# Kernel tuning notes

Hardware: AMD Instinct MI355X
Metric: run time of the kernel (lower is better)

Reference implementation:

```python
import jax, jax.numpy as jnp
import numpy as np

D_MODEL = 1024
NUM_HEADS = 16
NUM_KV_HEADS = 4
D_K = D_MODEL // NUM_HEADS  # 64
GROUP = NUM_HEADS // NUM_KV_HEADS  # 4
ROPE_BASE = 10000.0
NEG = -10000.0


def _rope_cos_sin(seq_len, d_k, dtype):
    # matches standard RotaryEmbedding: inv_freq over even dims, emb = cat(freqs, freqs)
    inv_freq = 1.0 / (ROPE_BASE ** (jnp.arange(0, d_k, 2, dtype=jnp.float32) / d_k))
    t = jnp.arange(seq_len, dtype=jnp.float32)
    freqs = jnp.einsum('s,f->sf', t, inv_freq)          # [S, d_k/2]
    emb = jnp.concatenate([freqs, freqs], axis=-1)       # [S, d_k]
    return jnp.cos(emb).astype(dtype), jnp.sin(emb).astype(dtype)


def _apply_rope(x, cos, sin):
    # x: [B, H, S, d_k]; cos/sin: [S, d_k] broadcast over B, H
    half = x.shape[-1] // 2
    x1, x2 = x[..., :half], x[..., half:]
    rotated = jnp.concatenate([-x2, x1], axis=-1)
    return x * cos + rotated * sin


def setup_inputs() -> dict:
    key = jax.random.key(0)
    ks = jax.random.split(key, 7)
    B, S = 2, 2048
    scale = 1.0 / np.sqrt(D_MODEL)
    return {
        'query': jax.random.normal(ks[0], (B, S, D_MODEL), dtype=jnp.float32),
        'key': jax.random.normal(ks[1], (B, S, D_MODEL), dtype=jnp.float32),
        'value': jax.random.normal(ks[2], (B, S, D_MODEL), dtype=jnp.float32),
        'Wq': jax.random.normal(ks[3], (D_MODEL, D_MODEL), dtype=jnp.float32) * scale,
        'Wk': jax.random.normal(ks[4], (NUM_KV_HEADS * D_K, D_MODEL), dtype=jnp.float32) * scale,
        'Wv': jax.random.normal(ks[5], (NUM_KV_HEADS * D_K, D_MODEL), dtype=jnp.float32) * scale,
        'Wo': jax.random.normal(ks[6], (D_MODEL, D_MODEL), dtype=jnp.float32) * scale,
    }


def reference(query, key, value, Wq, Wk, Wv, Wo):
    B, Sq, _ = query.shape
    Sk = key.shape[1]
    # projections (nn.Linear: x @ W.T)
    Q = (query @ Wq.T).reshape(B, Sq, NUM_HEADS, D_K).transpose(0, 2, 1, 3)      # [B,H,Sq,dk]
    K = (key @ Wk.T).reshape(B, Sk, NUM_KV_HEADS, D_K).transpose(0, 2, 1, 3)      # [B,Hkv,Sk,dk]
    V = (value @ Wv.T).reshape(B, Sk, NUM_KV_HEADS, D_K).transpose(0, 2, 1, 3)    # [B,Hkv,Sk,dk]
    # RoPE
    cos, sin = _rope_cos_sin(Sq, D_K, Q.dtype)
    Q = _apply_rope(Q, cos, sin)
    K = _apply_rope(K, cos[:Sk], sin[:Sk])
    # GQA attention without explicitly materializing expanded K/V:
    # group query heads as [B, Hkv, G, Sq, dk]
    Qg = Q.reshape(B, NUM_KV_HEADS, GROUP, Sq, D_K)
    scores = jnp.einsum('bhgqd,bhkd->bhgqk', Qg, K) / jnp.sqrt(jnp.float32(D_K))  # [B,Hkv,G,Sq,Sk]
    causal = jnp.tril(jnp.ones((Sq, Sk), dtype=bool))
    scores = jnp.where(causal, scores, jnp.float32(NEG))
    probs = jax.nn.softmax(scores, axis=-1)
    out = jnp.einsum('bhgqk,bhkd->bhgqd', probs, V)                                # [B,Hkv,G,Sq,dk]
    out = out.reshape(B, NUM_HEADS, Sq, D_K).transpose(0, 2, 1, 3).reshape(B, Sq, D_MODEL)
    return out @ Wo.T
```

## Files before the change

### kernel.cpp

```cpp
#include <hip/hip_runtime.h>
#include <hip/hip_bf16.h>
#include <stdint.h>

typedef __attribute__((ext_vector_type(4))) float f32x4;
typedef __attribute__((ext_vector_type(8))) short short8;

#define S_LEN 2048
#define BATCH 2
#define NH 16
#define NKV 4
#define DK 64

__device__ __forceinline__ ushort f2bf(float f) {
  __hip_bfloat16 h = __float2bfloat16(f);
  ushort u; __builtin_memcpy(&u, &h, 2); return u;
}
__device__ __forceinline__ float bf2f(ushort h) {
  union { uint32_t u; float f; } v; v.u = ((uint32_t)h) << 16;
  return v.f;
}

__device__ __forceinline__ void gld16(const void* g, void* l) {
  __builtin_amdgcn_global_load_lds((const __attribute__((address_space(1))) void*)g,
                                   (__attribute__((address_space(3))) void*)l,
                                   16, 0, 0);
}

template<int CTRL>
__device__ __forceinline__ float dpp_movf(float x) {
  return __int_as_float(__builtin_amdgcn_update_dpp(0, __float_as_int(x), CTRL, 0xF, 0xF, true));
}
__device__ __forceinline__ float rowred_sum16(float v) {
  v += dpp_movf<0xB1>(v);
  v += dpp_movf<0x4E>(v);
  v += dpp_movf<0x141>(v);
  v += dpp_movf<0x140>(v);
  return v;
}

__global__ void preproc_kernel(const float* __restrict__ w0, const float* __restrict__ w1,
                               const float* __restrict__ w2, const float* __restrict__ w3,
                               ushort* __restrict__ o0, ushort* __restrict__ o1,
                               ushort* __restrict__ o2, ushort* __restrict__ o3,
                               float* __restrict__ tab) {
  const int y = blockIdx.y, tid = threadIdx.x;
  if (y < 4) {
    int n4 = (y == 0 || y == 3) ? 262144 : 65536;
    int i = (blockIdx.x << 8) + tid;
    if (i >= n4) return;
    const float* in = y == 0 ? w0 : y == 1 ? w1 : y == 2 ? w2 : w3;
    ushort* out = y == 0 ? o0 : y == 1 ? o1 : y == 2 ? o2 : o3;
    float4 x = ((const float4*)in)[i];
    ushort4 o;
    o.x = f2bf(x.x); o.y = f2bf(x.y); o.z = f2bf(x.z); o.w = f2bf(x.w);
    ((ushort4*)out)[i] = o;
  } else {
    int j = (blockIdx.x << 8) + tid;
    if (j >= 65536) return;
    int s = j >> 5, f = j & 31;
    float freq = (float)s * powf(10000.0f, -(float)f / 32.0f);
    tab[j] = cosf(freq);
    tab[65536 + j] = sinf(freq);
  }
}

template<int EPI, int AF32>
__device__ __forceinline__ void gemm_body(const void* __restrict__ Avp,
                                          const ushort* __restrict__ W,
                                          void* __restrict__ Cout,
                                          const float* __restrict__ tab,
                                          int N, int K, int bx, int by,
                                          void* AlV, ushort* Wl) {
  const int t = threadIdx.x;
  const int lane = t & 63;
  const int w = t >> 6;
  const int wr = w >> 1, wc = w & 1;
  const int m0 = bx * 64, n0 = by * 128;
  const int g = lane >> 4, q16 = lane & 15;

  f32x4 acc[2][4] = {};

  const int lrow = lane >> 2, lcol = (lane & 3) * 8;
  const int r8 = lane >> 3, c8 = lane & 7;

  const ushort* Wp0 = W + (size_t)(n0 + w * 32 + lrow) * K + lcol;
  const ushort* Wp1 = W + (size_t)(n0 + w * 32 + 16 + lrow) * K + lcol;
  ushort* Wb0 = &Wl[(w * 32) * 32];
  ushort* Wb1 = &Wl[(w * 32 + 16) * 32];

  const ushort* Ab16 = nullptr; const float* Af32 = nullptr;
  if (AF32) Af32 = (const float*)Avp; else Ab16 = (const ushort*)Avp;

  const int KSTEPS = K >> 5;
  for (int kt = 0; kt < KSTEPS; ++kt) {
    const int k0 = kt << 5;
    __syncthreads();
    if (AF32) {
      float* Alf = (float*)AlV;
      #pragma unroll
      for (int c = 0; c < 2; ++c) {
        int call = w * 2 + c;
        int row = call * 8 + r8;
        gld16(Af32 + (size_t)(m0 + row) * K + k0 + ((c8 ^ r8) << 2),
              Alf + (size_t)call * 272);
      }
    } else {
      ushort* Alh = (ushort*)AlV;
      gld16(Ab16 + (size_t)(m0 + w * 16 + lrow) * K + k0 + lcol,
            Alh + (size_t)(w * 16) * 32);
    }
    gld16(Wp0 + k0, Wb0);
    gld16(Wp1 + k0, Wb1);
    __syncthreads();
    short8 af[2], wf[4];
    #pragma unroll
    for (int i = 0; i < 2; ++i) {
      int row = wr * 32 + i * 16 + q16;
      if (AF32) {
        const float* Alf = (const float*)AlV;
        int fbase = (row >> 3) * 272 + (row & 7) * 32;
        int s0 = (g * 2) ^ (q16 & 7), s1 = (g * 2 + 1) ^ (q16 & 7);
        float4 v0 = *(const float4*)&Alf[fbase + s0 * 4];
        float4 v1 = *(const float4*)&Alf[fbase + s1 * 4];
        short8 a;
        a[0] = (short)f2bf(v0.x); a[1] = (short)f2bf(v0.y);
        a[2] = (short)f2bf(v0.z); a[3] = (short)f2bf(v0.w);
        a[4] = (short)f2bf(v1.x); a[5] = (short)f2bf(v1.y);
        a[6] = (short)f2bf(v1.z); a[7] = (short)f2bf(v1.w);
        af[i] = a;
      } else {
        const ushort* Alh = (const ushort*)AlV;
        af[i] = *(const short8*)&Alh[row * 32 + g * 8];
      }
    }
    #pragma unroll
    for (int j = 0; j < 4; ++j)
      wf[j] = *(const short8*)&Wl[(wc * 64 + j * 16 + q16) * 32 + g * 8];
    #pragma unroll
    for (int i = 0; i < 2; ++i)
      #pragma unroll
      for (int j = 0; j < 4; ++j)
        acc[i][j] = __builtin_amdgcn_mfma_f32_16x16x32_bf16(af[i], wf[j], acc[i][j], 0, 0, 0);
  }

  if (EPI == 0) {
    #pragma unroll
    for (int i = 0; i < 2; ++i)
      #pragma unroll
      for (int j = 0; j < 4; ++j) {
        int row0 = m0 + wr * 32 + i * 16 + g * 4;
        int col  = n0 + wc * 64 + j * 16 + q16;
        #pragma unroll
        for (int r = 0; r < 4; ++r)
          ((float*)Cout)[(size_t)(row0 + r) * N + col] = acc[i][j][r];
      }
  } else if (EPI == 1 || EPI == 2) {
    const int NHE = (EPI == 1) ? NH : NKV;
    const float qscale = (EPI == 1) ? 0.125f : 1.0f;
    const int h = (n0 + wc * 64) >> 6;
    ushort* O = (ushort*)Cout;
    #pragma unroll
    for (int i = 0; i < 2; ++i)
      #pragma unroll
      for (int j = 0; j < 2; ++j) {
        const int d = j * 16 + q16;
        #pragma unroll
        for (int r = 0; r < 4; ++r) {
          int row = m0 + wr * 32 + i * 16 + g * 4 + r;
          int b = row >> 11, s = row & 2047;
          float x1 = acc[i][j][r], x2 = acc[i][j + 2][r];
          float c = tab[s * 32 + d], sn = tab[65536 + s * 32 + d];
          ushort* base = O + ((size_t)(b * NHE + h) * 2048 + s) * 64;
          base[d]      = f2bf((x1 * c - x2 * sn) * qscale);
          base[d + 32] = f2bf((x2 * c + x1 * sn) * qscale);
        }
      }
  } else {
    const int h = (n0 + wc * 64) >> 6;
    ushort* O = (ushort*)Cout;
    #pragma unroll
    for (int i = 0; i < 2; ++i) {
      int row0 = m0 + wr * 32 + i * 16 + g * 4;
      int b = row0 >> 11, s0 = row0 & 2047;
      #pragma unroll
      for (int j = 0; j < 4; ++j) {
        const int d = j * 16 + q16;
        ushort4 o;
        o.x = f2bf(acc[i][j][0]); o.y = f2bf(acc[i][j][1]);
        o.z = f2bf(acc[i][j][2]); o.w = f2bf(acc[i][j][3]);
        *(ushort4*)(O + ((size_t)(b * NKV + h) * 64 + d) * 2048 + s0) = o;
      }
    }
  }
}

__global__ __launch_bounds__(256) void qkv_gemm_kernel(
    const float* __restrict__ query, const ushort* __restrict__ wqb, ushort* __restrict__ Qh,
    const float* __restrict__ key,   const ushort* __restrict__ wkb, ushort* __restrict__ Kh,
    const float* __restrict__ value, const ushort* __restrict__ wvb, ushort* __restrict__ Vt,
    const float* __restrict__ tab) {
  __shared__ float Al[8 * 272];
  __shared__ ushort Wl[128 * 32];
  const int id = blockIdx.x;
  if (id < 128) {
    gemm_body<2, 1>(key, wkb, Kh, tab, 256, 1024, id & 63, id >> 6, Al, Wl);
  } else if (id < 256) {
    const int i = id - 128;
    gemm_body<3, 1>(value, wvb, Vt, tab, 256, 1024, i & 63, i >> 6, Al, Wl);
  } else {
    const int i = id - 256;
    gemm_body<1, 1>(query, wqb, Qh, tab, 1024, 1024, i & 63, i >> 6, Al, Wl);
  }
}

__global__ __launch_bounds__(256) void o_gemm_kernel(const ushort* __restrict__ AO,
                                                     const ushort* __restrict__ wob,
                                                     float* __restrict__ out) {
  __shared__ ushort Al[64 * 32];
  __shared__ ushort Wl[128 * 32];
  gemm_body<0, 0>(AO, wob, out, nullptr, 1024, 1024, blockIdx.x & 63, blockIdx.x >> 6, Al, Wl);
}

__global__ __launch_bounds__(256) void fattn_kernel(const ushort* __restrict__ Qh,
                                                    const ushort* __restrict__ Kh,
                                                    const ushort* __restrict__ Vt,
                                                    ushort* __restrict__ AO) {
  __shared__ ushort Klds[2][4096];
  __shared__ ushort Vlds[2][4096];
  __shared__ ushort Plds[4][1024];
  const int t = threadIdx.x, lane = t & 63, wv = t >> 6;
  const int g = lane >> 4, q16 = lane & 15;

  const int hh = blockIdx.y;
  const int b = hh >> 4, h = hh & 15;
  const int kvh = h >> 2;
  const ushort* Kbase = Kh + (size_t)(b * 4 + kvh) * 2048 * 64;
  const ushort* Vbase = Vt + (size_t)(b * 4 + kvh) * 64 * 2048;

  const int r3 = lane >> 3, c3 = lane & 7;
  const int swz = (c3 ^ r3) << 3;
  const int call0 = wv * 2;

  for (int pass = 0; pass < 2; ++pass) {
    const int qt = pass ? (31 - (int)blockIdx.x) : (int)blockIdx.x;
    const int q0 = qt * 64 + wv * 16;
    const ushort* Qbase = Qh + ((size_t)hh * 2048 + q0) * 64;

    short8 aq[2];
    aq[0] = *(const short8*)(Qbase + (size_t)q16 * 64 + g * 8);
    aq[1] = *(const short8*)(Qbase + (size_t)q16 * 64 + 32 + g * 8);

    f32x4 acc[4] = {};
    float lsum[4] = {0.f, 0.f, 0.f, 0.f};

    const int nkb = qt + 1;

    __syncthreads();
    #pragma unroll
    for (int c = 0; c < 2; ++c) {
      int call = call0 + c;
      int row = call * 8 + r3;
      gld16(Kbase + (size_t)row * 64 + swz, &Klds[0][call * 512]);
      gld16(Vbase + (size_t)row * 2048 + swz, &Vlds[0][call * 512]);
    }

    int buf = 0;
    for (int kb = 0; kb < nkb; ++kb) {
      __syncthreads();
      if (kb + 1 < nkb) {
        const int k0n = (kb + 1) * 64;
        #pragma unroll
        for (int c = 0; c < 2; ++c) {
          int call = call0 + c;
          int row = call * 8 + r3;
          gld16(Kbase + (size_t)(k0n + row) * 64 + swz, &Klds[buf ^ 1][call * 512]);
          gld16(Vbase + (size_t)row * 2048 + k0n + swz, &Vlds[buf ^ 1][call * 512]);
        }
      }
      const ushort* Kl = Klds[buf];
      const ushort* Vl = Vlds[buf];
      const int k0 = kb * 64;

      f32x4 sA[4] = {};
      __builtin_amdgcn_s_setprio(1);
      #pragma unroll
      for (int kk = 0; kk < 2; ++kk)
        #pragma unroll
        for (int nt = 0; nt < 4; ++nt) {
          int row = nt * 16 + q16;
          int slot = ((kk << 2) | g) ^ (q16 & 7);
          short8 bk = *(const short8*)(Kl + row * 64 + (slot << 3));
          sA[nt] = __builtin_amdgcn_mfma_f32_16x16x32_bf16(aq[kk], bk, sA[nt], 0, 0, 0);
        }
      __builtin_amdgcn_s_setprio(0);

      if (kb == nkb - 1) {
        #pragma unroll
        for (int nt = 0; nt < 4; ++nt)
          #pragma unroll
          for (int r = 0; r < 4; ++r) {
            int col = k0 + nt * 16 + q16, row = q0 + g * 4 + r;
            if (col > row) sA[nt][r] = -1e30f;
          }
      }

      float ps[4][4];
      #pragma unroll
      for (int nt = 0; nt < 4; ++nt)
        #pragma unroll
        for (int r = 0; r < 4; ++r)
          ps[nt][r] = __expf(sA[nt][r]);
      #pragma unroll
      for (int r = 0; r < 4; ++r)
        lsum[r] += (ps[0][r] + ps[1][r]) + (ps[2][r] + ps[3][r]);

      #pragma unroll
      for (int nt = 0; nt < 4; ++nt)
        #pragma unroll
        for (int r = 0; r < 4; ++r) {
          int pr = g * 4 + r;
          Plds[wv][pr * 64 + ((nt * 16 + q16) ^ ((pr & 7) << 3))] = f2bf(ps[nt][r]);
        }
      __builtin_amdgcn_s_setprio(1);
      #pragma unroll
      for (int kk2 = 0; kk2 < 2; ++kk2) {
        int slot = ((kk2 << 2) | g) ^ (q16 & 7);
        short8 pa = *(const short8*)(&Plds[wv][q16 * 64 + (slot << 3)]);
        #pragma unroll
        for (int dt = 0; dt < 4; ++dt) {
          int rv = dt * 16 + q16;
          short8 bv = *(const short8*)(Vl + rv * 64 + (slot << 3));
          acc[dt] = __builtin_amdgcn_mfma_f32_16x16x32_bf16(pa, bv, acc[dt], 0, 0, 0);
        }
      }
      __builtin_amdgcn_s_setprio(0);

      buf ^= 1;
    }

    float linv[4];
    #pragma unroll
    for (int r = 0; r < 4; ++r) linv[r] = 1.0f / rowred_sum16(lsum[r]);
    #pragma unroll
    for (int dt = 0; dt < 4; ++dt)
      #pragma unroll
      for (int r = 0; r < 4; ++r) {
        float o = acc[dt][r] * linv[r];
        AO[((size_t)(b * 2048) + q0 + g * 4 + r) * 1024 + h * 64 + dt * 16 + q16] = f2bf(o);
      }
  }
}

extern "C" void kernel_launch(void* const* d_in, const int* in_sizes, int n_in,
                              void* d_out, int out_size, void* d_ws, size_t ws_size,
                              hipStream_t stream) {
  const float* query = (const float*)d_in[0];
  const float* key   = (const float*)d_in[1];
  const float* value = (const float*)d_in[2];
  const float* Wq    = (const float*)d_in[3];
  const float* Wk    = (const float*)d_in[4];
  const float* Wv    = (const float*)d_in[5];
  const float* Wo    = (const float*)d_in[6];
  float* out = (float*)d_out;

  char* ws = (char*)d_ws;
  size_t off = 0;
  auto alloc = [&](size_t bytes) {
    void* p = ws + off; off += (bytes + 255) & ~255ULL; return p;
  };
  ushort* wqb = (ushort*)alloc(1024ULL * 1024 * 2);
  ushort* wkb = (ushort*)alloc(256ULL * 1024 * 2);
  ushort* wvb = (ushort*)alloc(256ULL * 1024 * 2);
  ushort* wob = (ushort*)alloc(1024ULL * 1024 * 2);
  ushort* Qh  = (ushort*)alloc(4096ULL * 1024 * 2);
  ushort* Kh  = (ushort*)alloc(4096ULL * 256 * 2);
  ushort* Vt  = (ushort*)alloc(4096ULL * 256 * 2);
  ushort* AO  = (ushort*)alloc(4096ULL * 1024 * 2);
  float*  tab = (float*)alloc(2048ULL * 32 * 4 * 2);

  preproc_kernel<<<dim3(1024, 5), 256, 0, stream>>>(Wq, Wk, Wv, Wo,
                                                    wqb, wkb, wvb, wob, (float*)tab);

  qkv_gemm_kernel<<<768, 256, 0, stream>>>(query, wqb, Qh, key, wkb, Kh,
                                           value, wvb, Vt, (float*)tab);

  fattn_kernel<<<dim3(16, 32), 256, 0, stream>>>(Qh, Kh, Vt, AO);

  o_gemm_kernel<<<512, 256, 0, stream>>>(AO, wob, out);
}
```

Measured before the change: 98.95 us.

## Give each attention wave two query subtiles and halve block size

Flash-attention blocks now use two waves of 128 threads instead of four, with each wave processing 32 query rows as two 16-row subtiles. Each K and V fragment read from LDS feeds two MFMAs, which cuts LDS reads per unit of compute and per-block load overhead. The trade-off is fewer waves resident per CU, giving less latency hiding, plus higher register pressure from the doubled accumulators.

```diff
diff --git a/kernel.cpp b/kernel.cpp
--- a/kernel.cpp
+++ b/kernel.cpp
@@ -221,13 +221,13 @@
   gemm_body<0, 0>(AO, wob, out, nullptr, 1024, 1024, blockIdx.x & 63, blockIdx.x >> 6, Al, Wl);
 }
 
-__global__ __launch_bounds__(256) void fattn_kernel(const ushort* __restrict__ Qh,
+__global__ __launch_bounds__(128) void fattn_kernel(const ushort* __restrict__ Qh,
                                                     const ushort* __restrict__ Kh,
                                                     const ushort* __restrict__ Vt,
                                                     ushort* __restrict__ AO) {
   __shared__ ushort Klds[2][4096];
   __shared__ ushort Vlds[2][4096];
-  __shared__ ushort Plds[4][1024];
+  __shared__ ushort Plds[2][2048];
   const int t = threadIdx.x, lane = t & 63, wv = t >> 6;
   const int g = lane >> 4, q16 = lane & 15;
 
@@ -239,25 +239,28 @@
 
   const int r3 = lane >> 3, c3 = lane & 7;
   const int swz = (c3 ^ r3) << 3;
-  const int call0 = wv * 2;
+  const int call0 = wv * 4;
 
   for (int pass = 0; pass < 2; ++pass) {
     const int qt = pass ? (31 - (int)blockIdx.x) : (int)blockIdx.x;
-    const int q0 = qt * 64 + wv * 16;
+    const int q0 = qt * 64 + wv * 32;
     const ushort* Qbase = Qh + ((size_t)hh * 2048 + q0) * 64;
 
-    short8 aq[2];
-    aq[0] = *(const short8*)(Qbase + (size_t)q16 * 64 + g * 8);
-    aq[1] = *(const short8*)(Qbase + (size_t)q16 * 64 + 32 + g * 8);
-
-    f32x4 acc[4] = {};
-    float lsum[4] = {0.f, 0.f, 0.f, 0.f};
+    short8 aq[2][2];
+    #pragma unroll
+    for (int sub = 0; sub < 2; ++sub)
+      #pragma unroll
+      for (int kk = 0; kk < 2; ++kk)
+        aq[sub][kk] = *(const short8*)(Qbase + (size_t)(sub * 16 + q16) * 64 + kk * 32 + g * 8);
+
+    f32x4 acc[2][4] = {};
+    float lsum[2][4] = {};
 
     const int nkb = qt + 1;
 
     __syncthreads();
     #pragma unroll
-    for (int c = 0; c < 2; ++c) {
+    for (int c = 0; c < 4; ++c) {
       int call = call0 + c;
       int row = call * 8 + r3;
       gld16(Kbase + (size_t)row * 64 + swz, &Klds[0][call * 512]);
@@ -270,7 +273,7 @@
       if (kb + 1 < nkb) {
         const int k0n = (kb + 1) * 64;
         #pragma unroll
-        for (int c = 0; c < 2; ++c) {
+        for (int c = 0; c < 4; ++c) {
           int call = call0 + c;
           int row = call * 8 + r3;
           gld16(Kbase + (size_t)(k0n + row) * 64 + swz, &Klds[buf ^ 1][call * 512]);
@@ -281,7 +284,7 @@
       const ushort* Vl = Vlds[buf];
       const int k0 = kb * 64;
 
-      f32x4 sA[4] = {};
+      f32x4 sA[2][4] = {};
       __builtin_amdgcn_s_setprio(1);
       #pragma unroll
       for (int kk = 0; kk < 2; ++kk)
@@ -290,47 +293,56 @@
           int row = nt * 16 + q16;
           int slot = ((kk << 2) | g) ^ (q16 & 7);
           short8 bk = *(const short8*)(Kl + row * 64 + (slot << 3));
-          sA[nt] = __builtin_amdgcn_mfma_f32_16x16x32_bf16(aq[kk], bk, sA[nt], 0, 0, 0);
+          sA[0][nt] = __builtin_amdgcn_mfma_f32_16x16x32_bf16(aq[0][kk], bk, sA[0][nt], 0, 0, 0);
+          sA[1][nt] = __builtin_amdgcn_mfma_f32_16x16x32_bf16(aq[1][kk], bk, sA[1][nt], 0, 0, 0);
         }
       __builtin_amdgcn_s_setprio(0);
 
       if (kb == nkb - 1) {
+        #pragma unroll
+        for (int sub = 0; sub < 2; ++sub)
+          #pragma unroll
+          for (int nt = 0; nt < 4; ++nt)
+            #pragma unroll
+            for (int r = 0; r < 4; ++r) {
+              int col = k0 + nt * 16 + q16, row = q0 + sub * 16 + g * 4 + r;
+              if (col > row) sA[sub][nt][r] = -1e30f;
+            }
+      }
+
+      #pragma unroll
+      for (int sub = 0; sub < 2; ++sub) {
+        #pragma unroll
+        for (int nt = 0; nt < 4; ++nt)
+          #pragma unroll
+          for (int r = 0; r < 4; ++r)
+            sA[sub][nt][r] = __expf(sA[sub][nt][r]);
+        #pragma unroll
+        for (int r = 0; r < 4; ++r)
+          lsum[sub][r] += (sA[sub][0][r] + sA[sub][1][r]) + (sA[sub][2][r] + sA[sub][3][r]);
+      }
+
+      #pragma unroll
+      for (int sub = 0; sub < 2; ++sub)
         #pragma unroll
         for (int nt = 0; nt < 4; ++nt)
           #pragma unroll
           for (int r = 0; r < 4; ++r) {
-            int col = k0 + nt * 16 + q16, row = q0 + g * 4 + r;
-            if (col > row) sA[nt][r] = -1e30f;
+            int pr = sub * 16 + g * 4 + r;
+            Plds[wv][pr * 64 + ((nt * 16 + q16) ^ ((pr & 7) << 3))] = f2bf(sA[sub][nt][r]);
           }
-      }
-
-      float ps[4][4];
-      #pragma unroll
-      for (int nt = 0; nt < 4; ++nt)
-        #pragma unroll
-        for (int r = 0; r < 4; ++r)
-          ps[nt][r] = __expf(sA[nt][r]);
-      #pragma unroll
-      for (int r = 0; r < 4; ++r)
-        lsum[r] += (ps[0][r] + ps[1][r]) + (ps[2][r] + ps[3][r]);
-
-      #pragma unroll
-      for (int nt = 0; nt < 4; ++nt)
-        #pragma unroll
-        for (int r = 0; r < 4; ++r) {
-          int pr = g * 4 + r;
-          Plds[wv][pr * 64 + ((nt * 16 + q16) ^ ((pr & 7) << 3))] = f2bf(ps[nt][r]);
-        }
       __builtin_amdgcn_s_setprio(1);
       #pragma unroll
       for (int kk2 = 0; kk2 < 2; ++kk2) {
         int slot = ((kk2 << 2) | g) ^ (q16 & 7);
-        short8 pa = *(const short8*)(&Plds[wv][q16 * 64 + (slot << 3)]);
+        short8 pa0 = *(const short8*)(&Plds[wv][(q16) * 64 + (slot << 3)]);
+        short8 pa1 = *(const short8*)(&Plds[wv][(16 + q16) * 64 + (slot << 3)]);
         #pragma unroll
         for (int dt = 0; dt < 4; ++dt) {
           int rv = dt * 16 + q16;
           short8 bv = *(const short8*)(Vl + rv * 64 + (slot << 3));
-          acc[dt] = __builtin_amdgcn_mfma_f32_16x16x32_bf16(pa, bv, acc[dt], 0, 0, 0);
+          acc[0][dt] = __builtin_amdgcn_mfma_f32_16x16x32_bf16(pa0, bv, acc[0][dt], 0, 0, 0);
+          acc[1][dt] = __builtin_amdgcn_mfma_f32_16x16x32_bf16(pa1, bv, acc[1][dt], 0, 0, 0);
         }
       }
       __builtin_amdgcn_s_setprio(0);
@@ -338,16 +350,19 @@
       buf ^= 1;
     }
 
-    float linv[4];
-    #pragma unroll
-    for (int r = 0; r < 4; ++r) linv[r] = 1.0f / rowred_sum16(lsum[r]);
-    #pragma unroll
-    for (int dt = 0; dt < 4; ++dt)
-      #pragma unroll
-      for (int r = 0; r < 4; ++r) {
-        float o = acc[dt][r] * linv[r];
-        AO[((size_t)(b * 2048) + q0 + g * 4 + r) * 1024 + h * 64 + dt * 16 + q16] = f2bf(o);
-      }
+    #pragma unroll
+    for (int sub = 0; sub < 2; ++sub) {
+      float linv[4];
+      #pragma unroll
+      for (int r = 0; r < 4; ++r) linv[r] = 1.0f / rowred_sum16(lsum[sub][r]);
+      #pragma unroll
+      for (int dt = 0; dt < 4; ++dt)
+        #pragma unroll
+        for (int r = 0; r < 4; ++r) {
+          float o = acc[sub][dt][r] * linv[r];
+          AO[((size_t)(b * 2048) + q0 + sub * 16 + g * 4 + r) * 1024 + h * 64 + dt * 16 + q16] = f2bf(o);
+        }
+    }
   }
 }
 
@@ -384,7 +399,7 @@
   qkv_gemm_kernel<<<768, 256, 0, stream>>>(query, wqb, Qh, key, wkb, Kh,
                                            value, wvb, Vt, (float*)tab);
 
-  fattn_kernel<<<dim3(16, 32), 256, 0, stream>>>(Qh, Kh, Vt, AO);
+  fattn_kernel<<<dim3(16, 32), 128, 0, stream>>>(Qh, Kh, Vt, AO);
 
   o_gemm_kernel<<<512, 256, 0, stream>>>(AO, wob, out);
 }
```

Measured after the change: 118.3 us. 1.2x slower.
